# Kernel tuning notes

Measured on AMD Instinct MI355X. Metric: run time of the kernel, lower is better.

## Reference

```python
import jax, jax.numpy as jnp
import numpy as np

N = 100000
E = 3200000
IN_C, HID_C, OUT_C = 128, 16, 1


def setup_inputs() -> dict:
    key = jax.random.key(0)
    k1, k2, k3, k4, k5, k6 = jax.random.split(key, 6)
    x = jax.random.normal(k1, (N, IN_C), dtype=jnp.float32)
    edge_index = jax.random.randint(k2, (2, E), 0, N, dtype=jnp.int64)
    # Glorot-style init like PyG GCNConv
    W1 = jax.random.normal(k3, (IN_C, HID_C), dtype=jnp.float32) / np.sqrt(IN_C)
    b1 = jnp.zeros((HID_C,), dtype=jnp.float32)
    W2 = jax.random.normal(k4, (HID_C, OUT_C), dtype=jnp.float32) / np.sqrt(HID_C)
    b2 = jnp.zeros((OUT_C,), dtype=jnp.float32)
    return {"x": x, "edge_index": edge_index, "W1": W1, "b1": b1, "W2": W2, "b2": b2}


def _gcn_conv(x, W, b, src, dst, norm):
    # Linear transform first (PyG default flow: transform then aggregate)
    h = x @ W                                  # [N, C_out]
    msg = h[src] * norm[:, None]               # gather + edge-wise scale, [E+N, C_out]
    out = jax.ops.segment_sum(msg, dst, num_segments=N)  # scatter-add, [N, C_out]
    return out + b


def reference(x, edge_index, W1, b1, W2, b2):
    # GCNConv: add self-loops, symmetric normalization D^-1/2 A D^-1/2
    loop = jnp.arange(N, dtype=edge_index.dtype)
    src = jnp.concatenate([edge_index[0], loop])   # [E+N]
    dst = jnp.concatenate([edge_index[1], loop])   # [E+N]
    deg = jax.ops.segment_sum(jnp.ones_like(dst, dtype=x.dtype), dst, num_segments=N)
    dinv = jnp.where(deg > 0, jax.lax.rsqrt(deg), 0.0)
    norm = dinv[src] * dinv[dst]                   # [E+N]

    h = _gcn_conv(x, W1, b1, src, dst, norm)
    h = jax.nn.relu(h)
    # dropout is identity in eval mode (training=False)
    h = _gcn_conv(h, W2, b2, src, dst, norm)
    return jax.nn.sigmoid(h).squeeze()             # [N]
```

## Files before the change

kernel.cpp:

```cpp
#include <hip/hip_runtime.h>
#include <hip/hip_bf16.h>
#include <math.h>

typedef unsigned int u32;

constexpr int N_NODES = 100000;
constexpr int N_EDGES = 3200000;
constexpr int IN_C    = 128;
constexpr int HID_C   = 16;

constexpr int BKT_SHIFT = 11;
constexpr int BKT_NODES = 1 << BKT_SHIFT;
constexpr int NB  = (N_NODES + BKT_NODES - 1) / BKT_NODES;
constexpr int CAP = 67000;
constexpr int EPB = N_EDGES / 256;
constexpr int MAXE = (EPB + 1023) / 1024;
constexpr int K_SEG = 16;
constexpr int QW = 4;

__global__ void k_zero(u32* __restrict__ cursor) {
    int i = threadIdx.x;
    if (i < NB) cursor[i] = 0u;
}

__global__ __launch_bounds__(1024) void k_bucket(const int* __restrict__ src,
                                                 const int* __restrict__ dst,
                                                 u32* __restrict__ cursor,
                                                 u32* __restrict__ barr) {
    __shared__ u32 cnt4[QW][NB];
    __shared__ u32 lpre4[QW][NB];
    __shared__ u32 cur4[QW][NB];
    __shared__ u32 gbase[NB];
    __shared__ u32 bstart[NB + 1];
    __shared__ u32 ents[EPB];
    const int e0 = blockIdx.x * EPB;
    const int q = threadIdx.x >> 8;
    u32 myD[MAXE], myS[MAXE];
#pragma unroll
    for (int i = 0; i < MAXE; ++i) {
        int r = threadIdx.x + i * 1024;
        if (r < EPB) { myD[i] = (u32)dst[e0 + r]; myS[i] = (u32)src[e0 + r]; }
        else myD[i] = 0xFFFFFFFFu;
    }
    for (int i = threadIdx.x; i < QW * NB; i += 1024) ((u32*)cnt4)[i] = 0u;
    __syncthreads();
#pragma unroll
    for (int i = 0; i < MAXE; ++i)
        if (myD[i] != 0xFFFFFFFFu) atomicAdd(&cnt4[q][myD[i] >> BKT_SHIFT], 1u);
    __syncthreads();
    if (threadIdx.x == 0) {
        u32 t = 0;
        for (int b = 0; b < NB; ++b) {
            bstart[b] = t;
            for (int qq = 0; qq < QW; ++qq) { lpre4[qq][b] = t; t += cnt4[qq][b]; }
        }
        bstart[NB] = t;
    }
    __syncthreads();
    if (threadIdx.x < NB)
        gbase[threadIdx.x] = atomicAdd(&cursor[threadIdx.x],
                                       bstart[threadIdx.x + 1] - bstart[threadIdx.x]);
    for (int i = threadIdx.x; i < QW * NB; i += 1024) ((u32*)cur4)[i] = ((u32*)lpre4)[i];
    __syncthreads();
#pragma unroll
    for (int i = 0; i < MAXE; ++i) {
        if (myD[i] == 0xFFFFFFFFu) continue;
        u32 b = myD[i] >> BKT_SHIFT;
        u32 pos = atomicAdd(&cur4[q][b], 1u);
        ents[pos] = ((myD[i] & (BKT_NODES - 1)) << 17) | myS[i];
    }
    __syncthreads();
    const int wv = threadIdx.x >> 6, ln = threadIdx.x & 63;
    for (int b = wv; b < NB; b += 16) {
        u32 s0 = bstart[b], s1 = bstart[b + 1], gb = gbase[b];
        for (u32 i = s0 + ln; i < s1; i += 64) {
            u32 off = gb + (i - s0);
            if (off < (u32)CAP) barr[(size_t)b * CAP + off] = ents[i];
        }
    }
}

__global__ __launch_bounds__(1024) void k_hist(const u32* __restrict__ barr,
                                               const u32* __restrict__ cursor,
                                               u32* __restrict__ seghist) {
    __shared__ u32 h[BKT_NODES];
    const int b = blockIdx.x / K_SEG, s = blockIdx.x % K_SEG;
    const u32 sz = min(cursor[b], (u32)CAP);
    for (int i = threadIdx.x; i < BKT_NODES; i += blockDim.x) h[i] = 0u;
    __syncthreads();
    const u32 e0 = sz * (u32)s / K_SEG, e1 = sz * (u32)(s + 1) / K_SEG;
    const u32* p = barr + (size_t)b * CAP;
    for (u32 e = e0 + threadIdx.x; e < e1; e += blockDim.x)
        atomicAdd(&h[p[e] >> 17], 1u);
    __syncthreads();
    u32* o = seghist + (size_t)(b * K_SEG + s) * BKT_NODES;
    for (int i = threadIdx.x; i < BKT_NODES; i += blockDim.x) o[i] = h[i];
}

__global__ __launch_bounds__(1024) void k_scan(u32* __restrict__ seghist,
                                               const u32* __restrict__ cursor,
                                               int* __restrict__ rowptr,
                                               float* __restrict__ dinv) {
    __shared__ u32 sa[BKT_NODES];
    __shared__ u32 wsum[16];
    __shared__ u32 s_bb;
    const int b = blockIdx.x;
    const int nbase = b << BKT_SHIFT;
    if (threadIdx.x == 0) {
        u32 t = 0;
        for (int q = 0; q < b; ++q) t += min(cursor[q], (u32)CAP);
        s_bb = t;
        if (b == NB - 1) rowptr[N_NODES] = (int)(t + min(cursor[b], (u32)CAP));
    }
    for (int n = threadIdx.x; n < BKT_NODES; n += 1024) {
        u32 t = 0;
#pragma unroll
        for (int s = 0; s < K_SEG; ++s) {
            size_t idx = (size_t)(b * K_SEG + s) * BKT_NODES + n;
            u32 v = seghist[idx];
            seghist[idx] = t;
            t += v;
        }
        sa[n] = t;
        if (nbase + n < N_NODES) dinv[nbase + n] = rsqrtf(1.0f + (float)t);
    }
    __syncthreads();
    const int lane = threadIdx.x & 63, wv = threadIdx.x >> 6;
    u32 v0 = sa[2 * threadIdx.x], v1 = sa[2 * threadIdx.x + 1];
    u32 p = v0 + v1;
    u32 ip = p;
#pragma unroll
    for (int off = 1; off < 64; off <<= 1) {
        u32 nv = __shfl_up(ip, off);
        if (lane >= off) ip += nv;
    }
    if (lane == 63) wsum[wv] = ip;
    __syncthreads();
    if (threadIdx.x < 16) {
        u32 wx = wsum[threadIdx.x];
#pragma unroll
        for (int off = 1; off < 16; off <<= 1) {
            u32 nv = __shfl_up(wx, off);
            if ((int)threadIdx.x >= off) wx += nv;
        }
        wsum[threadIdx.x] = wx;
    }
    __syncthreads();
    u32 wbase = wv ? wsum[wv - 1] : 0u;
    u32 epair = wbase + ip - p;
    sa[2 * threadIdx.x]     = epair + v0;
    sa[2 * threadIdx.x + 1] = epair + p;
    __syncthreads();
    const u32 bb = s_bb;
    for (int n = threadIdx.x; n < BKT_NODES; n += 1024) {
        u32 excl = bb + (n ? sa[n - 1] : 0u);
        if (nbase + n < N_NODES) rowptr[nbase + n] = (int)excl;
#pragma unroll
        for (int s = 0; s < K_SEG; ++s)
            seghist[(size_t)(b * K_SEG + s) * BKT_NODES + n] += excl;
    }
}

__global__ __launch_bounds__(1024) void k_scatter(const u32* __restrict__ barr,
                                                  const u32* __restrict__ cursor,
                                                  const u32* __restrict__ seghist,
                                                  int* __restrict__ adj) {
    __shared__ u32 cur[BKT_NODES];
    const int b = blockIdx.x / K_SEG, s = blockIdx.x % K_SEG;
    const u32 sz = min(cursor[b], (u32)CAP);
    const u32* sbase = seghist + (size_t)(b * K_SEG + s) * BKT_NODES;
    for (int i = threadIdx.x; i < BKT_NODES; i += blockDim.x) cur[i] = sbase[i];
    __syncthreads();
    const u32 e0 = sz * (u32)s / K_SEG, e1 = sz * (u32)(s + 1) / K_SEG;
    const u32* p = barr + (size_t)b * CAP;
    for (u32 e = e0 + threadIdx.x; e < e1; e += blockDim.x) {
        u32 ent = p[e];
        u32 pos = atomicAdd(&cur[ent >> 17], 1u);
        adj[pos] = (int)(ent & 0x1FFFFu);
    }
}

constexpr int NPB = 16;
constexpr int XPAD = 132;
__global__ __launch_bounds__(256) void k_gemm1(const float* __restrict__ x,
                                               const float* __restrict__ W1,
                                               const float* __restrict__ dinv,
                                               __hip_bfloat16* __restrict__ g1b) {
    __shared__ float sx[NPB * XPAD];
    __shared__ float swT[HID_C * XPAD];
    const int nbase = blockIdx.x * NPB;
    {
        const float4* xs = (const float4*)(x + (size_t)nbase * IN_C);
#pragma unroll
        for (int k = 0; k < 2; ++k) {
            int idx = threadIdx.x + k * 256;
            int row = idx >> 5, col4 = idx & 31;
            float4 v = xs[idx];
            ((float4*)(sx + row * XPAD))[col4] = v;
        }
    }
    for (int t = threadIdx.x; t < IN_C * HID_C; t += 256) {
        int j = t >> 4, c = t & 15;
        swT[c * XPAD + j] = W1[t];
    }
    __syncthreads();

    const int n = threadIdx.x >> 4;
    const int c = threadIdx.x & 15;
    const float4* row = (const float4*)(sx + n * XPAD);
    const float4* wc  = (const float4*)(swT + c * XPAD);
    float acc = 0.f;
#pragma unroll
    for (int j = 0; j < IN_C / 4; ++j) {
        float4 v = row[j];
        float4 w = wc[j];
        acc = fmaf(v.x, w.x, acc);
        acc = fmaf(v.y, w.y, acc);
        acc = fmaf(v.z, w.z, acc);
        acc = fmaf(v.w, w.w, acc);
    }
    const int node = nbase + n;
    g1b[node * HID_C + c] = __float2bfloat16(acc * dinv[node]);
}

__global__ void k_agg1(const int* __restrict__ rowptr, const int* __restrict__ adj,
                       const uint4* __restrict__ g1q,
                       const float* __restrict__ dinv, const float* __restrict__ b1,
                       const float* __restrict__ W2, float* __restrict__ g2) {
    int t = blockIdx.x * blockDim.x + threadIdx.x;
    int g = t >> 1, l = t & 1;
    if (g >= N_NODES) return;
    int base = rowptr[g], end = rowptr[g + 1];
    float a0, a1, a2, a3, a4, a5, a6, a7;
    {
        uint4 sv = g1q[g * 2 + l];
        a0 = __uint_as_float(sv.x << 16);
        a1 = __uint_as_float(sv.x & 0xFFFF0000u);
        a2 = __uint_as_float(sv.y << 16);
        a3 = __uint_as_float(sv.y & 0xFFFF0000u);
        a4 = __uint_as_float(sv.z << 16);
        a5 = __uint_as_float(sv.z & 0xFFFF0000u);
        a6 = __uint_as_float(sv.w << 16);
        a7 = __uint_as_float(sv.w & 0xFFFF0000u);
    }
    int k = base;
    for (; k + 4 <= end; k += 4) {
        int s0 = adj[k], s1 = adj[k + 1], s2 = adj[k + 2], s3 = adj[k + 3];
        uint4 v0 = g1q[s0 * 2 + l], v1 = g1q[s1 * 2 + l];
        uint4 v2 = g1q[s2 * 2 + l], v3 = g1q[s3 * 2 + l];
        a0 += __uint_as_float(v0.x << 16);
        a1 += __uint_as_float(v0.x & 0xFFFF0000u);
        a2 += __uint_as_float(v0.y << 16);
        a3 += __uint_as_float(v0.y & 0xFFFF0000u);
        a4 += __uint_as_float(v0.z << 16);
        a5 += __uint_as_float(v0.z & 0xFFFF0000u);
        a6 += __uint_as_float(v0.w << 16);
        a7 += __uint_as_float(v0.w & 0xFFFF0000u);
        a0 += __uint_as_float(v1.x << 16);
        a1 += __uint_as_float(v1.x & 0xFFFF0000u);
        a2 += __uint_as_float(v1.y << 16);
        a3 += __uint_as_float(v1.y & 0xFFFF0000u);
        a4 += __uint_as_float(v1.z << 16);
        a5 += __uint_as_float(v1.z & 0xFFFF0000u);
        a6 += __uint_as_float(v1.w << 16);
        a7 += __uint_as_float(v1.w & 0xFFFF0000u);
        a0 += __uint_as_float(v2.x << 16);
        a1 += __uint_as_float(v2.x & 0xFFFF0000u);
        a2 += __uint_as_float(v2.y << 16);
        a3 += __uint_as_float(v2.y & 0xFFFF0000u);
        a4 += __uint_as_float(v2.z << 16);
        a5 += __uint_as_float(v2.z & 0xFFFF0000u);
        a6 += __uint_as_float(v2.w << 16);
        a7 += __uint_as_float(v2.w & 0xFFFF0000u);
        a0 += __uint_as_float(v3.x << 16);
        a1 += __uint_as_float(v3.x & 0xFFFF0000u);
        a2 += __uint_as_float(v3.y << 16);
        a3 += __uint_as_float(v3.y & 0xFFFF0000u);
        a4 += __uint_as_float(v3.z << 16);
        a5 += __uint_as_float(v3.z & 0xFFFF0000u);
        a6 += __uint_as_float(v3.w << 16);
        a7 += __uint_as_float(v3.w & 0xFFFF0000u);
    }
    for (; k < end; ++k) {
        uint4 v = g1q[adj[k] * 2 + l];
        a0 += __uint_as_float(v.x << 16);
        a1 += __uint_as_float(v.x & 0xFFFF0000u);
        a2 += __uint_as_float(v.y << 16);
        a3 += __uint_as_float(v.y & 0xFFFF0000u);
        a4 += __uint_as_float(v.z << 16);
        a5 += __uint_as_float(v.z & 0xFFFF0000u);
        a6 += __uint_as_float(v.w << 16);
        a7 += __uint_as_float(v.w & 0xFFFF0000u);
    }
    float di = dinv[g];
    float4 bA = ((const float4*)b1)[2 * l], bB = ((const float4*)b1)[2 * l + 1];
    float4 wA = ((const float4*)W2)[2 * l], wB = ((const float4*)W2)[2 * l + 1];
    float h0 = fmaxf(fmaf(a0, di, bA.x), 0.f);
    float h1 = fmaxf(fmaf(a1, di, bA.y), 0.f);
    float h2 = fmaxf(fmaf(a2, di, bA.z), 0.f);
    float h3 = fmaxf(fmaf(a3, di, bA.w), 0.f);
    float h4 = fmaxf(fmaf(a4, di, bB.x), 0.f);
    float h5 = fmaxf(fmaf(a5, di, bB.y), 0.f);
    float h6 = fmaxf(fmaf(a6, di, bB.z), 0.f);
    float h7 = fmaxf(fmaf(a7, di, bB.w), 0.f);
    float part = h0 * wA.x + h1 * wA.y + h2 * wA.z + h3 * wA.w
               + h4 * wB.x + h5 * wB.y + h6 * wB.z + h7 * wB.w;
    part += __shfl_xor(part, 1);
    if (l == 0) g2[g] = part * di;
}

__global__ void k_agg2(const int* __restrict__ rowptr, const int* __restrict__ adj,
                       const float* __restrict__ g2, const float* __restrict__ dinv,
                       const float* __restrict__ b2, float* __restrict__ out) {
    int t = blockIdx.x * blockDim.x + threadIdx.x;
    int g = t >> 2, l = t & 3;
    if (g >= N_NODES) return;
    int base = rowptr[g], end = rowptr[g + 1];
    float acc = (l == 0) ? g2[g] : 0.f;
    for (int k = base + l; k < end; k += 4) acc += g2[adj[k]];
    acc += __shfl_xor(acc, 1);
    acc += __shfl_xor(acc, 2);
    if (l == 0) {
        float v = fmaf(acc, dinv[g], b2[0]);
        out[g] = 1.0f / (1.0f + __expf(-v));
    }
}

extern "C" void kernel_launch(void* const* d_in, const int* in_sizes, int n_in,
                              void* d_out, int out_size, void* d_ws, size_t ws_size,
                              hipStream_t stream) {
    const float* x    = (const float*)d_in[0];
    const int*   edge = (const int*)d_in[1];
    const float* b1   = (const float*)d_in[3];
    const float* W1   = (const float*)d_in[2];
    const float* W2   = (const float*)d_in[4];
    const float* b2   = (const float*)d_in[5];
    float*       out  = (float*)d_out;

    const int* src = edge;
    const int* dst = edge + N_EDGES;

    char* w = (char*)d_ws;
    auto alloc = [&](size_t bytes) { char* r = w; w += (bytes + 255) & ~(size_t)255; return r; };
    u32*   barr       = (u32*)  alloc((size_t)NB * CAP * 4);
    u32*   seghist    = (u32*)  alloc((size_t)NB * K_SEG * BKT_NODES * 4);
    u32*   cursor     = (u32*)  alloc(NB * 4);
    int*   rowptr     = (int*)  alloc((size_t)(N_NODES + 1) * 4);
    float* dinv       = (float*)alloc((size_t)N_NODES * 4);
    int*   adj        = (int*)  alloc((size_t)N_EDGES * 4);
    float*          g2  = (float*)barr;
    __hip_bfloat16* g1b = (__hip_bfloat16*)seghist;
    const uint4*    g1q = (const uint4*)seghist;

    const int gGemm = N_NODES / NPB;
    const int gAgg1 = (N_NODES * 2 + 255) / 256;
    const int gAgg2 = (N_NODES * 4 + 255) / 256;

    hipLaunchKernelGGL(k_zero,    dim3(1),          dim3(64),   0, stream, cursor);
    hipLaunchKernelGGL(k_bucket,  dim3(256),        dim3(1024), 0, stream, src, dst, cursor, barr);
    hipLaunchKernelGGL(k_hist,    dim3(NB * K_SEG), dim3(1024), 0, stream, barr, cursor, seghist);
    hipLaunchKernelGGL(k_scan,    dim3(NB),         dim3(1024), 0, stream, seghist, cursor, rowptr, dinv);
    hipLaunchKernelGGL(k_scatter, dim3(NB * K_SEG), dim3(1024), 0, stream, barr, cursor, seghist, adj);
    hipLaunchKernelGGL(k_gemm1,   dim3(gGemm),      dim3(256),  0, stream, x, W1, dinv, g1b);
    hipLaunchKernelGGL(k_agg1,    dim3(gAgg1),      dim3(256),  0, stream, rowptr, adj, g1q, dinv, b1, W2, g2);
    hipLaunchKernelGGL(k_agg2,    dim3(gAgg2),      dim3(256),  0, stream, rowptr, adj, g2, dinv, b2, out);
}
```

Baseline: 232.9 us.

## Replace three-pass CSR build with fine buckets and single-block shared-memory sort

The CSR construction now uses 196 smaller buckets of 512 nodes each. One block per bucket builds the histogram, scans it, writes rowptr and dinv, sorts the entries in shared memory and writes adj out coalesced. This replaces the separate hist, scan and scatter kernels and the seghist global buffer, removing two launches and extra global traffic. The bucketing pass uses 128 blocks of 25000 edges, so each block holds 100KB of shared memory for its entries and occupancy is low. The bucket capacity of 17408 assumes roughly uniform destination degrees.

New measurement: 207.9 us. -10.8%, faster.

```diff
diff --git a/kernel.cpp b/kernel.cpp
--- a/kernel.cpp
+++ b/kernel.cpp
@@ -9,175 +9,121 @@
 constexpr int IN_C    = 128;
 constexpr int HID_C   = 16;
 
-constexpr int BKT_SHIFT = 11;
-constexpr int BKT_NODES = 1 << BKT_SHIFT;
-constexpr int NB  = (N_NODES + BKT_NODES - 1) / BKT_NODES;
-constexpr int CAP = 67000;
-constexpr int EPB = N_EDGES / 256;
-constexpr int MAXE = (EPB + 1023) / 1024;
-constexpr int K_SEG = 16;
-constexpr int QW = 4;
+constexpr int SB_SHIFT = 9;
+constexpr int SBN = 1 << SB_SHIFT;
+constexpr int NSB = (N_NODES + SBN - 1) / SBN;
+constexpr int CAP2 = 17408;
+constexpr int NBB = 128;
+constexpr int EPB = N_EDGES / NBB;
 
 __global__ void k_zero(u32* __restrict__ cursor) {
-    int i = threadIdx.x;
-    if (i < NB) cursor[i] = 0u;
+    int i = blockIdx.x * blockDim.x + threadIdx.x;
+    if (i < NSB) cursor[i] = 0u;
 }
 
 __global__ __launch_bounds__(1024) void k_bucket(const int* __restrict__ src,
                                                  const int* __restrict__ dst,
                                                  u32* __restrict__ cursor,
                                                  u32* __restrict__ barr) {
-    __shared__ u32 cnt4[QW][NB];
-    __shared__ u32 lpre4[QW][NB];
-    __shared__ u32 cur4[QW][NB];
-    __shared__ u32 gbase[NB];
-    __shared__ u32 bstart[NB + 1];
+    __shared__ u32 cnt[NSB];
+    __shared__ u32 bs[256];
+    __shared__ u32 cur[NSB];
+    __shared__ u32 gbase[NSB];
     __shared__ u32 ents[EPB];
     const int e0 = blockIdx.x * EPB;
-    const int q = threadIdx.x >> 8;
-    u32 myD[MAXE], myS[MAXE];
-#pragma unroll
-    for (int i = 0; i < MAXE; ++i) {
-        int r = threadIdx.x + i * 1024;
-        if (r < EPB) { myD[i] = (u32)dst[e0 + r]; myS[i] = (u32)src[e0 + r]; }
-        else myD[i] = 0xFFFFFFFFu;
-    }
-    for (int i = threadIdx.x; i < QW * NB; i += 1024) ((u32*)cnt4)[i] = 0u;
-    __syncthreads();
-#pragma unroll
-    for (int i = 0; i < MAXE; ++i)
-        if (myD[i] != 0xFFFFFFFFu) atomicAdd(&cnt4[q][myD[i] >> BKT_SHIFT], 1u);
-    __syncthreads();
-    if (threadIdx.x == 0) {
-        u32 t = 0;
-        for (int b = 0; b < NB; ++b) {
-            bstart[b] = t;
-            for (int qq = 0; qq < QW; ++qq) { lpre4[qq][b] = t; t += cnt4[qq][b]; }
-        }
-        bstart[NB] = t;
-    }
-    __syncthreads();
-    if (threadIdx.x < NB)
-        gbase[threadIdx.x] = atomicAdd(&cursor[threadIdx.x],
-                                       bstart[threadIdx.x + 1] - bstart[threadIdx.x]);
-    for (int i = threadIdx.x; i < QW * NB; i += 1024) ((u32*)cur4)[i] = ((u32*)lpre4)[i];
-    __syncthreads();
-#pragma unroll
-    for (int i = 0; i < MAXE; ++i) {
-        if (myD[i] == 0xFFFFFFFFu) continue;
-        u32 b = myD[i] >> BKT_SHIFT;
-        u32 pos = atomicAdd(&cur4[q][b], 1u);
-        ents[pos] = ((myD[i] & (BKT_NODES - 1)) << 17) | myS[i];
-    }
-    __syncthreads();
-    const int wv = threadIdx.x >> 6, ln = threadIdx.x & 63;
-    for (int b = wv; b < NB; b += 16) {
-        u32 s0 = bstart[b], s1 = bstart[b + 1], gb = gbase[b];
+    const int tid = threadIdx.x;
+    for (int i = tid; i < NSB; i += 1024) cnt[i] = 0u;
+    __syncthreads();
+    for (int e = e0 + tid; e < e0 + EPB; e += 1024)
+        atomicAdd(&cnt[((u32)dst[e]) >> SB_SHIFT], 1u);
+    __syncthreads();
+    if (tid < 256) bs[tid] = (tid < NSB) ? cnt[tid] : 0u;
+    __syncthreads();
+    for (int off = 1; off < 256; off <<= 1) {
+        u32 v = 0, a = 0;
+        if (tid < 256) { v = bs[tid]; if (tid >= off) a = bs[tid - off]; }
+        __syncthreads();
+        if (tid < 256) bs[tid] = v + a;
+        __syncthreads();
+    }
+    if (tid < NSB) {
+        gbase[tid] = atomicAdd(&cursor[tid], cnt[tid]);
+        cur[tid] = tid ? bs[tid - 1] : 0u;
+    }
+    __syncthreads();
+    for (int e = e0 + tid; e < e0 + EPB; e += 1024) {
+        u32 d = (u32)dst[e];
+        u32 b = d >> SB_SHIFT;
+        u32 pos = atomicAdd(&cur[b], 1u);
+        ents[pos] = ((d & (SBN - 1)) << 17) | (u32)src[e];
+    }
+    __syncthreads();
+    const int wv = tid >> 6, ln = tid & 63;
+    for (int b = wv; b < NSB; b += 16) {
+        u32 s0 = b ? bs[b - 1] : 0u, s1 = bs[b], gb = gbase[b];
         for (u32 i = s0 + ln; i < s1; i += 64) {
             u32 off = gb + (i - s0);
-            if (off < (u32)CAP) barr[(size_t)b * CAP + off] = ents[i];
+            if (off < (u32)CAP2) barr[(size_t)b * CAP2 + off] = ents[i];
         }
     }
 }
 
-__global__ __launch_bounds__(1024) void k_hist(const u32* __restrict__ barr,
-                                               const u32* __restrict__ cursor,
-                                               u32* __restrict__ seghist) {
-    __shared__ u32 h[BKT_NODES];
-    const int b = blockIdx.x / K_SEG, s = blockIdx.x % K_SEG;
-    const u32 sz = min(cursor[b], (u32)CAP);
-    for (int i = threadIdx.x; i < BKT_NODES; i += blockDim.x) h[i] = 0u;
-    __syncthreads();
-    const u32 e0 = sz * (u32)s / K_SEG, e1 = sz * (u32)(s + 1) / K_SEG;
-    const u32* p = barr + (size_t)b * CAP;
-    for (u32 e = e0 + threadIdx.x; e < e1; e += blockDim.x)
-        atomicAdd(&h[p[e] >> 17], 1u);
-    __syncthreads();
-    u32* o = seghist + (size_t)(b * K_SEG + s) * BKT_NODES;
-    for (int i = threadIdx.x; i < BKT_NODES; i += blockDim.x) o[i] = h[i];
-}
-
-__global__ __launch_bounds__(1024) void k_scan(u32* __restrict__ seghist,
+__global__ __launch_bounds__(1024) void k_sort(const u32* __restrict__ barr,
                                                const u32* __restrict__ cursor,
                                                int* __restrict__ rowptr,
-                                               float* __restrict__ dinv) {
-    __shared__ u32 sa[BKT_NODES];
-    __shared__ u32 wsum[16];
-    __shared__ u32 s_bb;
+                                               float* __restrict__ dinv,
+                                               int* __restrict__ adj) {
+    __shared__ u32 h[SBN];
+    __shared__ u32 ebase[SBN];
+    __shared__ u32 sc[256];
+    __shared__ u32 sorted[CAP2];
     const int b = blockIdx.x;
-    const int nbase = b << BKT_SHIFT;
-    if (threadIdx.x == 0) {
-        u32 t = 0;
-        for (int q = 0; q < b; ++q) t += min(cursor[q], (u32)CAP);
-        s_bb = t;
-        if (b == NB - 1) rowptr[N_NODES] = (int)(t + min(cursor[b], (u32)CAP));
-    }
-    for (int n = threadIdx.x; n < BKT_NODES; n += 1024) {
-        u32 t = 0;
-#pragma unroll
-        for (int s = 0; s < K_SEG; ++s) {
-            size_t idx = (size_t)(b * K_SEG + s) * BKT_NODES + n;
-            u32 v = seghist[idx];
-            seghist[idx] = t;
-            t += v;
+    const int tid = threadIdx.x;
+    const int nbase = b << SB_SHIFT;
+    if (tid < 256) sc[tid] = (tid < NSB) ? min(cursor[tid], (u32)CAP2) : 0u;
+    __syncthreads();
+    for (int off = 1; off < 256; off <<= 1) {
+        u32 v = 0, a = 0;
+        if (tid < 256) { v = sc[tid]; if (tid >= off) a = sc[tid - off]; }
+        __syncthreads();
+        if (tid < 256) sc[tid] = v + a;
+        __syncthreads();
+    }
+    const u32 sbbase = b ? sc[b - 1] : 0u;
+    const u32 sz = sc[b] - sbbase;
+    if (b == NSB - 1 && tid == 0) rowptr[N_NODES] = (int)sc[NSB - 1];
+    for (int i = tid; i < SBN; i += 1024) h[i] = 0u;
+    __syncthreads();
+    const u32* p = barr + (size_t)b * CAP2;
+    for (u32 e = tid; e < sz; e += 1024)
+        atomicAdd(&h[p[e] >> 17], 1u);
+    __syncthreads();
+    u32 myc = (tid < SBN) ? h[tid] : 0u;
+    for (int off = 1; off < SBN; off <<= 1) {
+        u32 v = 0, a = 0;
+        if (tid < SBN) { v = h[tid]; if (tid >= off) a = h[tid - off]; }
+        __syncthreads();
+        if (tid < SBN) h[tid] = v + a;
+        __syncthreads();
+    }
+    if (tid < SBN) {
+        u32 excl = h[tid] - myc;
+        ebase[tid] = excl;
+        int node = nbase + tid;
+        if (node < N_NODES) {
+            rowptr[node] = (int)(sbbase + excl);
+            dinv[node] = rsqrtf(1.0f + (float)myc);
         }
-        sa[n] = t;
-        if (nbase + n < N_NODES) dinv[nbase + n] = rsqrtf(1.0f + (float)t);
-    }
-    __syncthreads();
-    const int lane = threadIdx.x & 63, wv = threadIdx.x >> 6;
-    u32 v0 = sa[2 * threadIdx.x], v1 = sa[2 * threadIdx.x + 1];
-    u32 p = v0 + v1;
-    u32 ip = p;
-#pragma unroll
-    for (int off = 1; off < 64; off <<= 1) {
-        u32 nv = __shfl_up(ip, off);
-        if (lane >= off) ip += nv;
-    }
-    if (lane == 63) wsum[wv] = ip;
-    __syncthreads();
-    if (threadIdx.x < 16) {
-        u32 wx = wsum[threadIdx.x];
-#pragma unroll
-        for (int off = 1; off < 16; off <<= 1) {
-            u32 nv = __shfl_up(wx, off);
-            if ((int)threadIdx.x >= off) wx += nv;
-        }
-        wsum[threadIdx.x] = wx;
-    }
-    __syncthreads();
-    u32 wbase = wv ? wsum[wv - 1] : 0u;
-    u32 epair = wbase + ip - p;
-    sa[2 * threadIdx.x]     = epair + v0;
-    sa[2 * threadIdx.x + 1] = epair + p;
-    __syncthreads();
-    const u32 bb = s_bb;
-    for (int n = threadIdx.x; n < BKT_NODES; n += 1024) {
-        u32 excl = bb + (n ? sa[n - 1] : 0u);
-        if (nbase + n < N_NODES) rowptr[nbase + n] = (int)excl;
-#pragma unroll
-        for (int s = 0; s < K_SEG; ++s)
-            seghist[(size_t)(b * K_SEG + s) * BKT_NODES + n] += excl;
-    }
-}
-
-__global__ __launch_bounds__(1024) void k_scatter(const u32* __restrict__ barr,
-                                                  const u32* __restrict__ cursor,
-                                                  const u32* __restrict__ seghist,
-                                                  int* __restrict__ adj) {
-    __shared__ u32 cur[BKT_NODES];
-    const int b = blockIdx.x / K_SEG, s = blockIdx.x % K_SEG;
-    const u32 sz = min(cursor[b], (u32)CAP);
-    const u32* sbase = seghist + (size_t)(b * K_SEG + s) * BKT_NODES;
-    for (int i = threadIdx.x; i < BKT_NODES; i += blockDim.x) cur[i] = sbase[i];
-    __syncthreads();
-    const u32 e0 = sz * (u32)s / K_SEG, e1 = sz * (u32)(s + 1) / K_SEG;
-    const u32* p = barr + (size_t)b * CAP;
-    for (u32 e = e0 + threadIdx.x; e < e1; e += blockDim.x) {
+    }
+    __syncthreads();
+    for (u32 e = tid; e < sz; e += 1024) {
         u32 ent = p[e];
-        u32 pos = atomicAdd(&cur[ent >> 17], 1u);
-        adj[pos] = (int)(ent & 0x1FFFFu);
-    }
+        u32 pos = atomicAdd(&ebase[ent >> 17], 1u);
+        sorted[pos] = ent & 0x1FFFFu;
+    }
+    __syncthreads();
+    for (u32 i = tid; i < sz; i += 1024)
+        adj[sbbase + i] = (int)sorted[i];
 }
 
 constexpr int NPB = 16;
@@ -331,8 +277,8 @@
                               hipStream_t stream) {
     const float* x    = (const float*)d_in[0];
     const int*   edge = (const int*)d_in[1];
+    const float* W1   = (const float*)d_in[2];
     const float* b1   = (const float*)d_in[3];
-    const float* W1   = (const float*)d_in[2];
     const float* W2   = (const float*)d_in[4];
     const float* b2   = (const float*)d_in[5];
     float*       out  = (float*)d_out;
@@ -342,26 +288,23 @@
 
     char* w = (char*)d_ws;
     auto alloc = [&](size_t bytes) { char* r = w; w += (bytes + 255) & ~(size_t)255; return r; };
-    u32*   barr       = (u32*)  alloc((size_t)NB * CAP * 4);
-    u32*   seghist    = (u32*)  alloc((size_t)NB * K_SEG * BKT_NODES * 4);
-    u32*   cursor     = (u32*)  alloc(NB * 4);
-    int*   rowptr     = (int*)  alloc((size_t)(N_NODES + 1) * 4);
-    float* dinv       = (float*)alloc((size_t)N_NODES * 4);
-    int*   adj        = (int*)  alloc((size_t)N_EDGES * 4);
-    float*          g2  = (float*)barr;
-    __hip_bfloat16* g1b = (__hip_bfloat16*)seghist;
-    const uint4*    g1q = (const uint4*)seghist;
+    u32*   barr   = (u32*)  alloc((size_t)NSB * CAP2 * 4);
+    u32*   cursor = (u32*)  alloc(NSB * 4);
+    int*   rowptr = (int*)  alloc((size_t)(N_NODES + 1) * 4);
+    float* dinv   = (float*)alloc((size_t)N_NODES * 4);
+    int*   adj    = (int*)  alloc((size_t)N_EDGES * 4);
+    __hip_bfloat16* g1b = (__hip_bfloat16*)barr;
+    const uint4*    g1q = (const uint4*)barr;
+    float*          g2  = (float*)(barr + (size_t)N_NODES * HID_C / 2);
 
     const int gGemm = N_NODES / NPB;
     const int gAgg1 = (N_NODES * 2 + 255) / 256;
     const int gAgg2 = (N_NODES * 4 + 255) / 256;
 
-    hipLaunchKernelGGL(k_zero,    dim3(1),          dim3(64),   0, stream, cursor);
-    hipLaunchKernelGGL(k_bucket,  dim3(256),        dim3(1024), 0, stream, src, dst, cursor, barr);
-    hipLaunchKernelGGL(k_hist,    dim3(NB * K_SEG), dim3(1024), 0, stream, barr, cursor, seghist);
-    hipLaunchKernelGGL(k_scan,    dim3(NB),         dim3(1024), 0, stream, seghist, cursor, rowptr, dinv);
-    hipLaunchKernelGGL(k_scatter, dim3(NB * K_SEG), dim3(1024), 0, stream, barr, cursor, seghist, adj);
-    hipLaunchKernelGGL(k_gemm1,   dim3(gGemm),      dim3(256),  0, stream, x, W1, dinv, g1b);
-    hipLaunchKernelGGL(k_agg1,    dim3(gAgg1),      dim3(256),  0, stream, rowptr, adj, g1q, dinv, b1, W2, g2);
-    hipLaunchKernelGGL(k_agg2,    dim3(gAgg2),      dim3(256),  0, stream, rowptr, adj, g2, dinv, b2, out);
-}
+    hipLaunchKernelGGL(k_zero,   dim3(1),      dim3(256),  0, stream, cursor);
+    hipLaunchKernelGGL(k_bucket, dim3(NBB),    dim3(1024), 0, stream, src, dst, cursor, barr);
+    hipLaunchKernelGGL(k_sort,   dim3(NSB),    dim3(1024), 0, stream, barr, cursor, rowptr, dinv, adj);
+    hipLaunchKernelGGL(k_gemm1,  dim3(gGemm),  dim3(256),  0, stream, x, W1, dinv, g1b);
+    hipLaunchKernelGGL(k_agg1,   dim3(gAgg1),  dim3(256),  0, stream, rowptr, adj, g1q, dinv, b1, W2, g2);
+    hipLaunchKernelGGL(k_agg2,   dim3(gAgg2),  dim3(256),  0, stream, rowptr, adj, g2, dinv, b2, out);
+}
```
